# Kernel optimization log

Measured on AMD Instinct MI355X. Metric: run time of the kernel, lower is better.

## Reference

```python
import jax, jax.numpy as jnp
import numpy as np

B, L, C, OUT = 32, 1024, 64, 64
BN_EPS = 1e-5  # PyTorch BatchNorm1d default


def setup_inputs() -> dict:
    key = jax.random.key(0)
    kH, kA, kW = jax.random.split(key, 3)
    H = jax.random.normal(kH, (B, L, C), dtype=jnp.float32)
    A = jax.random.uniform(kA, (B, L, L), dtype=jnp.float32)  # positive degrees
    gamma = jnp.ones((C,), jnp.float32)
    beta = jnp.zeros((C,), jnp.float32)
    W = jax.random.normal(kW, (C, OUT), dtype=jnp.float32) * 0.05
    b = jnp.zeros((OUT,), jnp.float32)
    return {"H": H, "A": A, "gamma": gamma, "beta": beta, "W": W, "b": b}


def reference(H, A, gamma, beta, W, b):
    batch, l, c = H.shape
    # BatchNorm1d in train mode over the flattened (batch*l, c) node axis,
    # biased variance as in PyTorch.
    Hf = H.reshape(batch * l, c)
    mean = Hf.mean(axis=0)
    var = jnp.mean((Hf - mean) ** 2, axis=0)
    Hn = ((Hf - mean) * jax.lax.rsqrt(var + BN_EPS) * gamma + beta).reshape(batch, l, c)
    # Degree normalization: diag(d^0.5) @ A @ diag(d^-0.5) done as row/col scaling
    # (same math as the original's dense diagonal matmuls).
    d = A.sum(axis=2)                                   # [batch, l]
    A_norm = jnp.sqrt(d)[:, :, None] * A * jax.lax.rsqrt(d)[:, None, :]
    A_hat = jnp.eye(l, dtype=A.dtype) - A_norm          # I - D^0.5 A D^-0.5
    # Linear then batched propagation, LeakyReLU (default slope 0.01).
    X = Hn @ W + b                                      # [batch, l, out]
    out = jnp.einsum('bij,bjo->bio', A_hat, X)
    return jax.nn.leaky_relu(out, negative_slope=0.01)
```

## Files before the change

kernel.cpp:

```cpp
#include <hip/hip_runtime.h>

#define NB 32
#define NL 1024
#define NC 64
#define NO 64
constexpr float BN_EPS = 1e-5f;

#define D_OFF 128
#define PART_OFF 32896
#define YT_OFF 131072

typedef short          s16x8 __attribute__((ext_vector_type(8)));
typedef float          f32x16 __attribute__((ext_vector_type(16)));
typedef float          f32x4  __attribute__((ext_vector_type(4)));

__device__ inline unsigned short f2bf(float f) {
    union { float f; unsigned u; } v; v.f = f;
    unsigned u = v.u + 0x7FFFu + ((v.u >> 16) & 1u);
    return (unsigned short)(u >> 16);
}

__device__ inline void gload16(const void* g, void* l) {
    __builtin_amdgcn_global_load_lds(
        (const __attribute__((address_space(1))) unsigned int*)g,
        (__attribute__((address_space(3))) unsigned int*)l, 16, 0, 0);
}

__device__ inline s16x8 cvt8(f32x4 lo, f32x4 hi) {
    union { unsigned int i[4]; s16x8 v; } u;
    asm("v_cvt_pk_bf16_f32 %0, %1, %2" : "=v"(u.i[0]) : "v"(lo.x), "v"(lo.y));
    asm("v_cvt_pk_bf16_f32 %0, %1, %2" : "=v"(u.i[1]) : "v"(lo.z), "v"(lo.w));
    asm("v_cvt_pk_bf16_f32 %0, %1, %2" : "=v"(u.i[2]) : "v"(hi.x), "v"(hi.y));
    asm("v_cvt_pk_bf16_f32 %0, %1, %2" : "=v"(u.i[3]) : "v"(hi.z), "v"(hi.w));
    return u.v;
}

__global__ __launch_bounds__(256) void deg_bn(
    const float* __restrict__ A, const float* __restrict__ H,
    float* __restrict__ ws) {
    __shared__ f32x4 smem4[3072];
    const int t = threadIdx.x;
    if (blockIdx.x < 1024) {
        const int lane = t & 63, w = t >> 6;
        const size_t row0 = (size_t)blockIdx.x * 32;
        const char* src = (const char*)A + row0 * 4096;
        const int lo = w * 4096 + lane * 16;
#define STG(bi, c) do {                                                        \
            char* d0 = (char*)smem4 + (bi) * 16384 + lo;                       \
            const char* s0 = src + (c) * 16384 + lo;                           \
            gload16(s0,        d0);                                            \
            gload16(s0 + 1024, d0 + 1024);                                     \
            gload16(s0 + 2048, d0 + 2048);                                     \
            gload16(s0 + 3072, d0 + 3072);                                     \
        } while (0)
        STG(0, 0); STG(1, 1); STG(2, 2);
        int cb = 0;
#pragma unroll 1
        for (int c = 0; c < 8; ++c) {
            if (c <= 5)      asm volatile("s_waitcnt vmcnt(8)" ::: "memory");
            else if (c == 6) asm volatile("s_waitcnt vmcnt(4)" ::: "memory");
            else             asm volatile("s_waitcnt vmcnt(0)" ::: "memory");
            __builtin_amdgcn_sched_barrier(0);
            const char* cbp = (const char*)smem4 + cb * 16384 + lo;
            float s = 0.f;
#pragma unroll
            for (int j = 0; j < 4; ++j) {
                f32x4 v = *(const f32x4*)(cbp + j * 1024);
                s += v.x + v.y + v.z + v.w;
            }
#pragma unroll
            for (int m = 32; m; m >>= 1) s += __shfl_xor(s, m, 64);
            if (lane == 0) ws[D_OFF + row0 + c * 4 + w] = s;
            __builtin_amdgcn_sched_barrier(0);
            if (c + 3 < 8) STG(cb, c + 3);
            cb = (cb == 2) ? 0 : cb + 1;
        }
#undef STG
    } else {
        const int bb = blockIdx.x - 1024;
        const float4* Hv = (const float4*)H + bb * 4096;
        float s0 = 0.f, s1 = 0.f, s2 = 0.f, s3 = 0.f;
        float q0 = 0.f, q1 = 0.f, q2 = 0.f, q3 = 0.f;
#pragma unroll 4
        for (int s = 0; s < 16; ++s) {
            float4 v = Hv[s * 256 + t];
            s0 += v.x; q0 += v.x * v.x;
            s1 += v.y; q1 += v.y * v.y;
            s2 += v.z; q2 += v.z * v.z;
            s3 += v.w; q3 += v.w * v.w;
        }
        float* part = (float*)smem4;
        part[t * 8 + 0] = s0; part[t * 8 + 1] = s1;
        part[t * 8 + 2] = s2; part[t * 8 + 3] = s3;
        part[t * 8 + 4] = q0; part[t * 8 + 5] = q1;
        part[t * 8 + 6] = q2; part[t * 8 + 7] = q3;
        __syncthreads();
        if (t < 64) {
            const int g = t >> 2, e = t & 3;
            float a = 0.f, a2 = 0.f;
#pragma unroll
            for (int k = 0; k < 16; ++k) {
                a  += part[(g + 16 * k) * 8 + e];
                a2 += part[(g + 16 * k) * 8 + 4 + e];
            }
            ws[PART_OFF + bb * 64 + t] = a;
            ws[PART_OFF + 128 * 64 + bb * 64 + t] = a2;
        }
    }
}

__global__ __launch_bounds__(256) void linear_xy(
    const float* __restrict__ H, const float* __restrict__ Wm,
    const float* __restrict__ bias, const float* __restrict__ gamma,
    const float* __restrict__ beta, const float* __restrict__ ws,
    float* __restrict__ X, unsigned short* __restrict__ Yt) {
    __shared__ float Hl[64 * 64];
    __shared__ float Wl[64 * 64];
    __shared__ unsigned short Wbf[64 * 64];
    __shared__ unsigned short ytile[64][66];
    __shared__ float ls[256], ls2[256];
    __shared__ float sscale[64], sshift[64], bp[64], sdl[64];
    const int b = blockIdx.x >> 4, ch = blockIdx.x & 15;
    const int r0g = b * NL + ch * 64;
    const int t = threadIdx.x, lane = t & 63, w = t >> 6;

    {
        const char* hsrc = (const char*)H + (size_t)r0g * 256;
#pragma unroll
        for (int i = 0; i < 4; ++i) {
            const int L = i * 4096 + t * 16;
            const int row = L >> 8, cb = L & 255;
            gload16(hsrc + (size_t)row * 256 + (cb ^ ((row & 7) << 4)),
                    (char*)Hl + L);
        }
    }
    {
        const float4* Wv = (const float4*)Wm;
        float4* Wd = (float4*)Wl;
#pragma unroll
        for (int k = 0; k < 4; ++k) Wd[t + k * 256] = Wv[t + k * 256];
    }
    if (t < 64) sdl[t] = rsqrtf(ws[D_OFF + r0g + t]);
    {
        const float* ps  = ws + PART_OFF;
        const float* ps2 = ws + PART_OFF + 128 * 64;
        const int c = t & 63, q = t >> 6;
        float s = 0.f, s2 = 0.f;
        for (int p = q * 32; p < q * 32 + 32; ++p) {
            s  += ps[p * 64 + c];
            s2 += ps2[p * 64 + c];
        }
        ls[t] = s; ls2[t] = s2;
    }
    __syncthreads();
    if (t < 64) {
        const int c = t;
        float T  = ls[c]  + ls[c + 64]  + ls[c + 128]  + ls[c + 192];
        float T2 = ls2[c] + ls2[c + 64] + ls2[c + 128] + ls2[c + 192];
        const float n = (float)(NB * NL);
        float mean = T / n;
        float var  = T2 / n - mean * mean;
        float sc = gamma[c] * rsqrtf(var + BN_EPS);
        sscale[c] = sc;
        sshift[c] = beta[c] - mean * sc;
    }
    __syncthreads();
    {
        float p = 0.f;
#pragma unroll
        for (int c0 = 0; c0 < 16; ++c0) {
            const int c = w * 16 + c0;
            p += sshift[c] * Wl[c * 64 + lane];
        }
        ls[t] = p;
    }
#pragma unroll
    for (int c0 = 0; c0 < 16; ++c0) {
        const int c = w * 16 + c0;
        const float v = sscale[c] * Wl[c * 64 + lane];
        *(unsigned short*)((char*)Wbf + ((lane * 128 + c * 2) ^ ((lane & 7) << 4)))
            = f2bf(v);
    }
    __syncthreads();
    if (t < 64) bp[t] = bias[t] + ls[t] + ls[t + 64] + ls[t + 128] + ls[t + 192];
    __syncthreads();

    const int wr0  = (w >> 1) * 32;
    const int wc0  = (w & 1) * 32;
    const int frow = wr0 + (lane & 31);
    const int fcol = wc0 + (lane & 31);
    const int khb  = (lane >> 5) * 16;
    const int kfh  = (lane >> 5) * 32;
    const int swA  = (frow & 7) << 4;
    const int swY  = (fcol & 7) << 4;
    f32x16 acc;
#pragma unroll
    for (int r = 0; r < 16; ++r) acc[r] = 0.f;
    const char* ab = (const char*)Hl;
    const char* wb = (const char*)Wbf;
#pragma unroll
    for (int ks = 0; ks < 4; ++ks) {
        const int b0 = frow * 256 + ks * 64 + kfh;
        f32x4 flo = *(const f32x4*)(ab + ((b0)      ^ swA));
        f32x4 fhi = *(const f32x4*)(ab + ((b0 + 16) ^ swA));
        s16x8 af = cvt8(flo, fhi);
        s16x8 bf = *(const s16x8*)(wb + ((fcol * 128 + ks * 32 + khb) ^ swY));
        acc = __builtin_amdgcn_mfma_f32_32x32x16_bf16(af, bf, acc, 0, 0, 0);
    }
#pragma unroll
    for (int reg = 0; reg < 16; ++reg) {
        const int row = wr0 + (reg & 3) + 8 * (reg >> 2) + 4 * (lane >> 5);
        const int col = wc0 + (lane & 31);
        const float x = acc[reg] + bp[col];
        X[(size_t)(r0g + row) * NO + col] = x;
        ytile[row][col] = f2bf(x * sdl[row]);
    }
    __syncthreads();
    char* ybase = (char*)Yt + (size_t)(b * 16 + ch) * 8192;
#pragma unroll
    for (int i2 = 0; i2 < 16; ++i2) {
        const int col = i2 * 4 + w;
        *(unsigned short*)(ybase + ((col * 128 + lane * 2) ^ ((col & 7) << 4))) =
            ytile[lane][col];
    }
}

__global__ __launch_bounds__(256) void prop_mfma(
    const float* __restrict__ A, const unsigned short* __restrict__ Yt,
    const float* __restrict__ dbuf, float* __restrict__ XO) {

    __shared__ float Abuf[2][64 * 64];
    __shared__ unsigned short Ybuf[2][64 * 64];
    __shared__ float sdl[64];

    const int b  = blockIdx.x >> 4;
    const int mt = blockIdx.x & 15;
    const int i0 = mt * 64;
    const char* Abase = (const char*)A + ((size_t)(b * NL + i0)) * 4096;
    const char* YbT   = (const char*)Yt + (size_t)b * 16 * 8192;

    const int t    = threadIdx.x;
    const int lane = t & 63;
    const int w    = t >> 6;

    if (t < 64) sdl[t] = sqrtf(dbuf[b * NL + i0 + t]);

    const int tr = t >> 4;
    const int tc = (t & 15) * 16;
    const char* As[4];
#pragma unroll
    for (int i = 0; i < 4; ++i) {
        const int row = i * 16 + tr;
        As[i] = Abase + (size_t)row * 4096 + (tc ^ ((row & 7) << 4));
    }
    const int yL0 = t * 16, yL1 = t * 16 + 4096;

    const int wr0  = (w >> 1) * 32;
    const int wc0  = (w & 1) * 32;
    const int frow = wr0 + (lane & 31);
    const int fcol = wc0 + (lane & 31);
    const int khb  = (lane >> 5) * 16;
    const int kfh  = (lane >> 5) * 32;
    const int swA  = (frow & 7) << 4;
    const int swY  = (fcol & 7) << 4;

    f32x16 acc;
#pragma unroll
    for (int r = 0; r < 16; ++r) acc[r] = 0.f;

#define STAGE(bi, kt) do {                                                     \
        char* ad = (char*)Abuf[bi];                                            \
        gload16(As[0] + (kt) * 256, ad + t * 16);                              \
        gload16(As[1] + (kt) * 256, ad + 4096  + t * 16);                      \
        gload16(As[2] + (kt) * 256, ad + 8192  + t * 16);                      \
        gload16(As[3] + (kt) * 256, ad + 12288 + t * 16);                      \
        const char* ys = YbT + (size_t)(kt) * 8192;                            \
        char* yd = (char*)Ybuf[bi];                                            \
        gload16(ys + yL0, yd + yL0);                                           \
        gload16(ys + yL1, yd + yL1);                                           \
    } while (0)

    STAGE(0, 0);
    __syncthreads();

#pragma unroll 1
    for (int kti = 0; kti < 16; ++kti) {
        const int nxt = kti + 1;
        if (nxt < 16) STAGE(nxt & 1, nxt);
        const char* ab  = (const char*)Abuf[kti & 1];
        const char* yb2 = (const char*)Ybuf[kti & 1];
#pragma unroll
        for (int ks = 0; ks < 4; ++ks) {
            const int b0 = frow * 256 + ks * 64 + kfh;
            f32x4 flo = *(const f32x4*)(ab + ((b0)      ^ swA));
            f32x4 fhi = *(const f32x4*)(ab + ((b0 + 16) ^ swA));
            s16x8 af = cvt8(flo, fhi);
            s16x8 bf = *(const s16x8*)(yb2 + ((fcol * 128 + ks * 32 + khb) ^ swY));
            acc = __builtin_amdgcn_mfma_f32_32x32x16_bf16(af, bf, acc, 0, 0, 0);
        }
        __syncthreads();
    }
#undef STAGE

#pragma unroll
    for (int reg = 0; reg < 16; ++reg) {
        int row = (reg & 3) + 8 * (reg >> 2) + 4 * (lane >> 5);
        int i   = i0 + wr0 + row;
        int col = wc0 + (lane & 31);
        size_t idx = ((size_t)(b * NL + i)) * NO + col;
        float x = XO[idx];
        float v = x - sdl[wr0 + row] * acc[reg];
        XO[idx] = v > 0.f ? v : 0.01f * v;
    }
}

extern "C" void kernel_launch(void* const* d_in, const int* in_sizes, int n_in,
                              void* d_out, int out_size, void* d_ws, size_t ws_size,
                              hipStream_t stream) {
    const float* H     = (const float*)d_in[0];
    const float* A     = (const float*)d_in[1];
    const float* gamma = (const float*)d_in[2];
    const float* beta  = (const float*)d_in[3];
    const float* Wm    = (const float*)d_in[4];
    const float* bias  = (const float*)d_in[5];
    float* out = (float*)d_out;
    float* ws  = (float*)d_ws;
    unsigned short* Yt = (unsigned short*)(ws + YT_OFF);

    deg_bn<<<1152, 256, 0, stream>>>(A, H, ws);
    linear_xy<<<512, 256, 0, stream>>>(H, Wm, bias, gamma, beta, ws, out, Yt);
    prop_mfma<<<512, 256, 0, stream>>>(A, Yt, ws + D_OFF, out);
}
```

Measured before the change: 61.10 us.

## Fuse three kernels into one cooperative kernel with grid syncs

Merges the degree/BN-statistics, linear, and propagation kernels into a single cooperative launch of 512 blocks, using grid-wide syncs between phases. This removes two kernel launch boundaries and their idle gaps. Each block now reduces 64 rows of A instead of 32 for the degree pass, and the first 128 blocks also compute the BN partials. The cost is grid-sync overhead, fewer blocks available for the bandwidth-bound degree pass, and a 52 KB shared buffer that may reduce occupancy.

Result: slower. 192.1 us (+214.3%).

```diff
diff --git a/kernel.cpp b/kernel.cpp
--- a/kernel.cpp
+++ b/kernel.cpp
@@ -1,4 +1,6 @@
 #include <hip/hip_runtime.h>
+#include <hip/hip_cooperative_groups.h>
+namespace cg = cooperative_groups;
 
 #define NB 32
 #define NL 1024
@@ -35,18 +37,23 @@
     return u.v;
 }
 
-__global__ __launch_bounds__(256) void deg_bn(
+__global__ __launch_bounds__(256) void gcn_fused(
     const float* __restrict__ A, const float* __restrict__ H,
-    float* __restrict__ ws) {
-    __shared__ f32x4 smem4[3072];
-    const int t = threadIdx.x;
-    if (blockIdx.x < 1024) {
-        const int lane = t & 63, w = t >> 6;
-        const size_t row0 = (size_t)blockIdx.x * 32;
+    const float* __restrict__ Wm, const float* __restrict__ bias,
+    const float* __restrict__ gamma, const float* __restrict__ beta,
+    float* __restrict__ ws, float* __restrict__ X,
+    unsigned short* __restrict__ Yt) {
+
+    __shared__ __align__(16) char smem[52480];
+    const int blk = blockIdx.x;
+    const int t = threadIdx.x, lane = t & 63, w = t >> 6;
+
+    {
+        const size_t row0 = (size_t)blk * 64;
         const char* src = (const char*)A + row0 * 4096;
         const int lo = w * 4096 + lane * 16;
 #define STG(bi, c) do {                                                        \
-            char* d0 = (char*)smem4 + (bi) * 16384 + lo;                       \
+            char* d0 = smem + (bi) * 16384 + lo;                               \
             const char* s0 = src + (c) * 16384 + lo;                           \
             gload16(s0,        d0);                                            \
             gload16(s0 + 1024, d0 + 1024);                                     \
@@ -56,12 +63,12 @@
         STG(0, 0); STG(1, 1); STG(2, 2);
         int cb = 0;
 #pragma unroll 1
-        for (int c = 0; c < 8; ++c) {
-            if (c <= 5)      asm volatile("s_waitcnt vmcnt(8)" ::: "memory");
-            else if (c == 6) asm volatile("s_waitcnt vmcnt(4)" ::: "memory");
+        for (int c = 0; c < 16; ++c) {
+            if (c <= 13)     asm volatile("s_waitcnt vmcnt(8)" ::: "memory");
+            else if (c == 14) asm volatile("s_waitcnt vmcnt(4)" ::: "memory");
             else             asm volatile("s_waitcnt vmcnt(0)" ::: "memory");
             __builtin_amdgcn_sched_barrier(0);
-            const char* cbp = (const char*)smem4 + cb * 16384 + lo;
+            const char* cbp = smem + cb * 16384 + lo;
             float s = 0.f;
 #pragma unroll
             for (int j = 0; j < 4; ++j) {
@@ -72,13 +79,15 @@
             for (int m = 32; m; m >>= 1) s += __shfl_xor(s, m, 64);
             if (lane == 0) ws[D_OFF + row0 + c * 4 + w] = s;
             __builtin_amdgcn_sched_barrier(0);
-            if (c + 3 < 8) STG(cb, c + 3);
+            if (c + 3 < 16) STG(cb, c + 3);
             cb = (cb == 2) ? 0 : cb + 1;
         }
 #undef STG
-    } else {
-        const int bb = blockIdx.x - 1024;
-        const float4* Hv = (const float4*)H + bb * 4096;
+    }
+    if (blk < 128) {
+        __syncthreads();
+        float* part = (float*)smem;
+        const float4* Hv = (const float4*)H + blk * 4096;
         float s0 = 0.f, s1 = 0.f, s2 = 0.f, s3 = 0.f;
         float q0 = 0.f, q1 = 0.f, q2 = 0.f, q3 = 0.f;
 #pragma unroll 4
@@ -89,7 +98,6 @@
             s2 += v.z; q2 += v.z * v.z;
             s3 += v.w; q3 += v.w * v.w;
         }
-        float* part = (float*)smem4;
         part[t * 8 + 0] = s0; part[t * 8 + 1] = s1;
         part[t * 8 + 2] = s2; part[t * 8 + 3] = s3;
         part[t * 8 + 4] = q0; part[t * 8 + 5] = q1;
@@ -103,214 +111,214 @@
                 a  += part[(g + 16 * k) * 8 + e];
                 a2 += part[(g + 16 * k) * 8 + 4 + e];
             }
-            ws[PART_OFF + bb * 64 + t] = a;
-            ws[PART_OFF + 128 * 64 + bb * 64 + t] = a2;
+            ws[PART_OFF + blk * 64 + t] = a;
+            ws[PART_OFF + 128 * 64 + blk * 64 + t] = a2;
         }
     }
-}
-
-__global__ __launch_bounds__(256) void linear_xy(
-    const float* __restrict__ H, const float* __restrict__ Wm,
-    const float* __restrict__ bias, const float* __restrict__ gamma,
-    const float* __restrict__ beta, const float* __restrict__ ws,
-    float* __restrict__ X, unsigned short* __restrict__ Yt) {
-    __shared__ float Hl[64 * 64];
-    __shared__ float Wl[64 * 64];
-    __shared__ unsigned short Wbf[64 * 64];
-    __shared__ unsigned short ytile[64][66];
-    __shared__ float ls[256], ls2[256];
-    __shared__ float sscale[64], sshift[64], bp[64], sdl[64];
-    const int b = blockIdx.x >> 4, ch = blockIdx.x & 15;
-    const int r0g = b * NL + ch * 64;
-    const int t = threadIdx.x, lane = t & 63, w = t >> 6;
+
+    cg::this_grid().sync();
 
     {
-        const char* hsrc = (const char*)H + (size_t)r0g * 256;
-#pragma unroll
-        for (int i = 0; i < 4; ++i) {
-            const int L = i * 4096 + t * 16;
-            const int row = L >> 8, cb = L & 255;
-            gload16(hsrc + (size_t)row * 256 + (cb ^ ((row & 7) << 4)),
-                    (char*)Hl + L);
-        }
-    }
-    {
-        const float4* Wv = (const float4*)Wm;
-        float4* Wd = (float4*)Wl;
-#pragma unroll
-        for (int k = 0; k < 4; ++k) Wd[t + k * 256] = Wv[t + k * 256];
-    }
-    if (t < 64) sdl[t] = rsqrtf(ws[D_OFF + r0g + t]);
-    {
-        const float* ps  = ws + PART_OFF;
-        const float* ps2 = ws + PART_OFF + 128 * 64;
-        const int c = t & 63, q = t >> 6;
-        float s = 0.f, s2 = 0.f;
-        for (int p = q * 32; p < q * 32 + 32; ++p) {
-            s  += ps[p * 64 + c];
-            s2 += ps2[p * 64 + c];
-        }
-        ls[t] = s; ls2[t] = s2;
-    }
-    __syncthreads();
-    if (t < 64) {
-        const int c = t;
-        float T  = ls[c]  + ls[c + 64]  + ls[c + 128]  + ls[c + 192];
-        float T2 = ls2[c] + ls2[c + 64] + ls2[c + 128] + ls2[c + 192];
-        const float n = (float)(NB * NL);
-        float mean = T / n;
-        float var  = T2 / n - mean * mean;
-        float sc = gamma[c] * rsqrtf(var + BN_EPS);
-        sscale[c] = sc;
-        sshift[c] = beta[c] - mean * sc;
-    }
-    __syncthreads();
-    {
-        float p = 0.f;
+        float* Hl            = (float*)(smem);
+        float* Wl            = (float*)(smem + 16384);
+        unsigned short* Wbf  = (unsigned short*)(smem + 32768);
+        typedef unsigned short ytrow[66];
+        ytrow* ytile         = (ytrow*)(smem + 40960);
+        float* ls            = (float*)(smem + 49408);
+        float* ls2           = (float*)(smem + 50432);
+        float* sscale        = (float*)(smem + 51456);
+        float* sshift        = (float*)(smem + 51712);
+        float* bp            = (float*)(smem + 51968);
+        float* sdl           = (float*)(smem + 52224);
+        const int b = blk >> 4, ch = blk & 15;
+        const int r0g = b * NL + ch * 64;
+
+        {
+            const char* hsrc = (const char*)H + (size_t)r0g * 256;
+#pragma unroll
+            for (int i = 0; i < 4; ++i) {
+                const int L = i * 4096 + t * 16;
+                const int row = L >> 8, cb2 = L & 255;
+                gload16(hsrc + (size_t)row * 256 + (cb2 ^ ((row & 7) << 4)),
+                        (char*)Hl + L);
+            }
+        }
+        {
+            const float4* Wv = (const float4*)Wm;
+            float4* Wd = (float4*)Wl;
+#pragma unroll
+            for (int k = 0; k < 4; ++k) Wd[t + k * 256] = Wv[t + k * 256];
+        }
+        if (t < 64) sdl[t] = rsqrtf(ws[D_OFF + r0g + t]);
+        {
+            const float* ps  = ws + PART_OFF;
+            const float* ps2 = ws + PART_OFF + 128 * 64;
+            const int c = t & 63, q = t >> 6;
+            float s = 0.f, s2 = 0.f;
+            for (int p = q * 32; p < q * 32 + 32; ++p) {
+                s  += ps[p * 64 + c];
+                s2 += ps2[p * 64 + c];
+            }
+            ls[t] = s; ls2[t] = s2;
+        }
+        __syncthreads();
+        if (t < 64) {
+            const int c = t;
+            float T  = ls[c]  + ls[c + 64]  + ls[c + 128]  + ls[c + 192];
+            float T2 = ls2[c] + ls2[c + 64] + ls2[c + 128] + ls2[c + 192];
+            const float n = (float)(NB * NL);
+            float mean = T / n;
+            float var  = T2 / n - mean * mean;
+            float sc = gamma[c] * rsqrtf(var + BN_EPS);
+            sscale[c] = sc;
+            sshift[c] = beta[c] - mean * sc;
+        }
+        __syncthreads();
+        {
+            float p = 0.f;
+#pragma unroll
+            for (int c0 = 0; c0 < 16; ++c0) {
+                const int c = w * 16 + c0;
+                p += sshift[c] * Wl[c * 64 + lane];
+            }
+            ls[t] = p;
+        }
 #pragma unroll
         for (int c0 = 0; c0 < 16; ++c0) {
             const int c = w * 16 + c0;
-            p += sshift[c] * Wl[c * 64 + lane];
-        }
-        ls[t] = p;
-    }
-#pragma unroll
-    for (int c0 = 0; c0 < 16; ++c0) {
-        const int c = w * 16 + c0;
-        const float v = sscale[c] * Wl[c * 64 + lane];
-        *(unsigned short*)((char*)Wbf + ((lane * 128 + c * 2) ^ ((lane & 7) << 4)))
-            = f2bf(v);
-    }
-    __syncthreads();
-    if (t < 64) bp[t] = bias[t] + ls[t] + ls[t + 64] + ls[t + 128] + ls[t + 192];
-    __syncthreads();
-
-    const int wr0  = (w >> 1) * 32;
-    const int wc0  = (w & 1) * 32;
-    const int frow = wr0 + (lane & 31);
-    const int fcol = wc0 + (lane & 31);
-    const int khb  = (lane >> 5) * 16;
-    const int kfh  = (lane >> 5) * 32;
-    const int swA  = (frow & 7) << 4;
-    const int swY  = (fcol & 7) << 4;
-    f32x16 acc;
-#pragma unroll
-    for (int r = 0; r < 16; ++r) acc[r] = 0.f;
-    const char* ab = (const char*)Hl;
-    const char* wb = (const char*)Wbf;
-#pragma unroll
-    for (int ks = 0; ks < 4; ++ks) {
-        const int b0 = frow * 256 + ks * 64 + kfh;
-        f32x4 flo = *(const f32x4*)(ab + ((b0)      ^ swA));
-        f32x4 fhi = *(const f32x4*)(ab + ((b0 + 16) ^ swA));
-        s16x8 af = cvt8(flo, fhi);
-        s16x8 bf = *(const s16x8*)(wb + ((fcol * 128 + ks * 32 + khb) ^ swY));
-        acc = __builtin_amdgcn_mfma_f32_32x32x16_bf16(af, bf, acc, 0, 0, 0);
-    }
-#pragma unroll
-    for (int reg = 0; reg < 16; ++reg) {
-        const int row = wr0 + (reg & 3) + 8 * (reg >> 2) + 4 * (lane >> 5);
-        const int col = wc0 + (lane & 31);
-        const float x = acc[reg] + bp[col];
-        X[(size_t)(r0g + row) * NO + col] = x;
-        ytile[row][col] = f2bf(x * sdl[row]);
-    }
-    __syncthreads();
-    char* ybase = (char*)Yt + (size_t)(b * 16 + ch) * 8192;
-#pragma unroll
-    for (int i2 = 0; i2 < 16; ++i2) {
-        const int col = i2 * 4 + w;
-        *(unsigned short*)(ybase + ((col * 128 + lane * 2) ^ ((col & 7) << 4))) =
-            ytile[lane][col];
-    }
-}
-
-__global__ __launch_bounds__(256) void prop_mfma(
-    const float* __restrict__ A, const unsigned short* __restrict__ Yt,
-    const float* __restrict__ dbuf, float* __restrict__ XO) {
-
-    __shared__ float Abuf[2][64 * 64];
-    __shared__ unsigned short Ybuf[2][64 * 64];
-    __shared__ float sdl[64];
-
-    const int b  = blockIdx.x >> 4;
-    const int mt = blockIdx.x & 15;
-    const int i0 = mt * 64;
-    const char* Abase = (const char*)A + ((size_t)(b * NL + i0)) * 4096;
-    const char* YbT   = (const char*)Yt + (size_t)b * 16 * 8192;
-
-    const int t    = threadIdx.x;
-    const int lane = t & 63;
-    const int w    = t >> 6;
-
-    if (t < 64) sdl[t] = sqrtf(dbuf[b * NL + i0 + t]);
-
-    const int tr = t >> 4;
-    const int tc = (t & 15) * 16;
-    const char* As[4];
-#pragma unroll
-    for (int i = 0; i < 4; ++i) {
-        const int row = i * 16 + tr;
-        As[i] = Abase + (size_t)row * 4096 + (tc ^ ((row & 7) << 4));
-    }
-    const int yL0 = t * 16, yL1 = t * 16 + 4096;
-
-    const int wr0  = (w >> 1) * 32;
-    const int wc0  = (w & 1) * 32;
-    const int frow = wr0 + (lane & 31);
-    const int fcol = wc0 + (lane & 31);
-    const int khb  = (lane >> 5) * 16;
-    const int kfh  = (lane >> 5) * 32;
-    const int swA  = (frow & 7) << 4;
-    const int swY  = (fcol & 7) << 4;
-
-    f32x16 acc;
-#pragma unroll
-    for (int r = 0; r < 16; ++r) acc[r] = 0.f;
-
-#define STAGE(bi, kt) do {                                                     \
-        char* ad = (char*)Abuf[bi];                                            \
-        gload16(As[0] + (kt) * 256, ad + t * 16);                              \
-        gload16(As[1] + (kt) * 256, ad + 4096  + t * 16);                      \
-        gload16(As[2] + (kt) * 256, ad + 8192  + t * 16);                      \
-        gload16(As[3] + (kt) * 256, ad + 12288 + t * 16);                      \
-        const char* ys = YbT + (size_t)(kt) * 8192;                            \
-        char* yd = (char*)Ybuf[bi];                                            \
-        gload16(ys + yL0, yd + yL0);                                           \
-        gload16(ys + yL1, yd + yL1);                                           \
-    } while (0)
-
-    STAGE(0, 0);
-    __syncthreads();
-
-#pragma unroll 1
-    for (int kti = 0; kti < 16; ++kti) {
-        const int nxt = kti + 1;
-        if (nxt < 16) STAGE(nxt & 1, nxt);
-        const char* ab  = (const char*)Abuf[kti & 1];
-        const char* yb2 = (const char*)Ybuf[kti & 1];
+            const float v = sscale[c] * Wl[c * 64 + lane];
+            *(unsigned short*)((char*)Wbf +
+                ((lane * 128 + c * 2) ^ ((lane & 7) << 4))) = f2bf(v);
+        }
+        __syncthreads();
+        if (t < 64) bp[t] = bias[t] + ls[t] + ls[t + 64] + ls[t + 128] + ls[t + 192];
+        __syncthreads();
+
+        const int wr0  = (w >> 1) * 32;
+        const int wc0  = (w & 1) * 32;
+        const int frow = wr0 + (lane & 31);
+        const int fcol = wc0 + (lane & 31);
+        const int khb  = (lane >> 5) * 16;
+        const int kfh  = (lane >> 5) * 32;
+        const int swA  = (frow & 7) << 4;
+        const int swY  = (fcol & 7) << 4;
+        f32x16 acc;
+#pragma unroll
+        for (int r = 0; r < 16; ++r) acc[r] = 0.f;
+        const char* ab = (const char*)Hl;
+        const char* wb = (const char*)Wbf;
 #pragma unroll
         for (int ks = 0; ks < 4; ++ks) {
             const int b0 = frow * 256 + ks * 64 + kfh;
             f32x4 flo = *(const f32x4*)(ab + ((b0)      ^ swA));
             f32x4 fhi = *(const f32x4*)(ab + ((b0 + 16) ^ swA));
             s16x8 af = cvt8(flo, fhi);
-            s16x8 bf = *(const s16x8*)(yb2 + ((fcol * 128 + ks * 32 + khb) ^ swY));
+            s16x8 bf = *(const s16x8*)(wb + ((fcol * 128 + ks * 32 + khb) ^ swY));
             acc = __builtin_amdgcn_mfma_f32_32x32x16_bf16(af, bf, acc, 0, 0, 0);
         }
-        __syncthreads();
+#pragma unroll
+        for (int reg = 0; reg < 16; ++reg) {
+            const int row = wr0 + (reg & 3) + 8 * (reg >> 2) + 4 * (lane >> 5);
+            const int col = wc0 + (lane & 31);
+            const float x = acc[reg] + bp[col];
+            X[(size_t)(r0g + row) * NO + col] = x;
+            ytile[row][col] = f2bf(x * sdl[row]);
+        }
+        __syncthreads();
+        char* ybase = (char*)Yt + (size_t)(b * 16 + ch) * 8192;
+#pragma unroll
+        for (int i2 = 0; i2 < 16; ++i2) {
+            const int col = i2 * 4 + w;
+            *(unsigned short*)(ybase +
+                ((col * 128 + lane * 2) ^ ((col & 7) << 4))) = ytile[lane][col];
+        }
     }
+
+    cg::this_grid().sync();
+
+    {
+        char* Ab0 = smem;
+        char* Ab1 = smem + 16384;
+        char* Yb0 = smem + 32768;
+        char* Yb1 = smem + 40960;
+        float* sdl = (float*)(smem + 49152);
+
+        const int b  = blk >> 4;
+        const int mt = blk & 15;
+        const int i0 = mt * 64;
+        const char* Abase = (const char*)A + ((size_t)(b * NL + i0)) * 4096;
+        const char* YbT   = (const char*)Yt + (size_t)b * 16 * 8192;
+
+        if (t < 64) sdl[t] = sqrtf(ws[D_OFF + b * NL + i0 + t]);
+
+        const int tr = t >> 4;
+        const int tc = (t & 15) * 16;
+        const char* As[4];
+#pragma unroll
+        for (int i = 0; i < 4; ++i) {
+            const int row = i * 16 + tr;
+            As[i] = Abase + (size_t)row * 4096 + (tc ^ ((row & 7) << 4));
+        }
+        const int yL0 = t * 16, yL1 = t * 16 + 4096;
+
+        const int wr0  = (w >> 1) * 32;
+        const int wc0  = (w & 1) * 32;
+        const int frow = wr0 + (lane & 31);
+        const int fcol = wc0 + (lane & 31);
+        const int khb  = (lane >> 5) * 16;
+        const int kfh  = (lane >> 5) * 32;
+        const int swA  = (frow & 7) << 4;
+        const int swY  = (fcol & 7) << 4;
+
+        f32x16 acc;
+#pragma unroll
+        for (int r = 0; r < 16; ++r) acc[r] = 0.f;
+
+#define STAGE(bi, kt) do {                                                     \
+            char* ad = (bi) ? Ab1 : Ab0;                                       \
+            gload16(As[0] + (kt) * 256, ad + t * 16);                          \
+            gload16(As[1] + (kt) * 256, ad + 4096  + t * 16);                  \
+            gload16(As[2] + (kt) * 256, ad + 8192  + t * 16);                  \
+            gload16(As[3] + (kt) * 256, ad + 12288 + t * 16);                  \
+            const char* ys = YbT + (size_t)(kt) * 8192;                        \
+            char* yd = (bi) ? Yb1 : Yb0;                                       \
+            gload16(ys + yL0, yd + yL0);                                       \
+            gload16(ys + yL1, yd + yL1);                                       \
+        } while (0)
+
+        STAGE(0, 0);
+        __syncthreads();
+
+#pragma unroll 1
+        for (int kti = 0; kti < 16; ++kti) {
+            const int nxt = kti + 1;
+            if (nxt < 16) STAGE(nxt & 1, nxt);
+            const char* ab  = (kti & 1) ? Ab1 : Ab0;
+            const char* yb2 = (kti & 1) ? Yb1 : Yb0;
+#pragma unroll
+            for (int ks = 0; ks < 4; ++ks) {
+                const int b0 = frow * 256 + ks * 64 + kfh;
+                f32x4 flo = *(const f32x4*)(ab + ((b0)      ^ swA));
+                f32x4 fhi = *(const f32x4*)(ab + ((b0 + 16) ^ swA));
+                s16x8 af = cvt8(flo, fhi);
+                s16x8 bf = *(const s16x8*)(yb2 +
+                               ((fcol * 128 + ks * 32 + khb) ^ swY));
+                acc = __builtin_amdgcn_mfma_f32_32x32x16_bf16(af, bf, acc, 0, 0, 0);
+            }
+            __syncthreads();
+        }
 #undef STAGE
 
 #pragma unroll
-    for (int reg = 0; reg < 16; ++reg) {
-        int row = (reg & 3) + 8 * (reg >> 2) + 4 * (lane >> 5);
-        int i   = i0 + wr0 + row;
-        int col = wc0 + (lane & 31);
-        size_t idx = ((size_t)(b * NL + i)) * NO + col;
-        float x = XO[idx];
-        float v = x - sdl[wr0 + row] * acc[reg];
-        XO[idx] = v > 0.f ? v : 0.01f * v;
+        for (int reg = 0; reg < 16; ++reg) {
+            int row = (reg & 3) + 8 * (reg >> 2) + 4 * (lane >> 5);
+            int i   = i0 + wr0 + row;
+            int col = wc0 + (lane & 31);
+            size_t idx = ((size_t)(b * NL + i)) * NO + col;
+            float x = X[idx];
+            float v = x - sdl[wr0 + row] * acc[reg];
+            X[idx] = v > 0.f ? v : 0.01f * v;
+        }
     }
 }
 
@@ -327,7 +335,9 @@
     float* ws  = (float*)d_ws;
     unsigned short* Yt = (unsigned short*)(ws + YT_OFF);
 
-    deg_bn<<<1152, 256, 0, stream>>>(A, H, ws);
-    linear_xy<<<512, 256, 0, stream>>>(H, Wm, bias, gamma, beta, ws, out, Yt);
-    prop_mfma<<<512, 256, 0, stream>>>(A, Yt, ws + D_OFF, out);
-}
+    void* args[] = {(void*)&A, (void*)&H, (void*)&Wm, (void*)&bias,
+                    (void*)&gamma, (void*)&beta, (void*)&ws, (void*)&out,
+                    (void*)&Yt};
+    hipLaunchCooperativeKernel((void*)gcn_fused, dim3(512), dim3(256),
+                               args, 0, stream);
+}
```
